# Optimization experiments

Hardware: AMD Instinct MI355X
Metric: run time of the kernel (lower is better)

The kernel has to match this reference:

```python
import jax, jax.numpy as jnp
import numpy as np

B, N, D, H = 256, 40, 256, 256      # molecules, atoms/molecule, pc_hidden, pred_hidden
nS, nC, nB = 40, 5, 5               # n_SYMBOLS, n_FORMAL_CHARGES, n_BOND_TYPES
NEG_SLOPE = 0.01                    # F.leaky_relu default


def _lrelu(x):
    return jnp.where(x >= 0, x, NEG_SLOPE * x)


def setup_inputs() -> dict:
    key = jax.random.key(0)
    ks = jax.random.split(key, 7)
    def w(k, shape, fan_in):
        return jax.random.normal(k, shape, jnp.float32) / np.float32(np.sqrt(fan_in))
    return {
        "yhat": jax.random.normal(ks[0], (B, N, D), jnp.float32),
        "Ws1": w(ks[1], (D, H), D),      "bs1": jnp.zeros((H,), jnp.float32),
        "Ws2": w(ks[2], (H, nS), H),     "bs2": jnp.zeros((nS,), jnp.float32),
        "Wc1": w(ks[3], (D, H), D),      "bc1": jnp.zeros((H,), jnp.float32),
        "Wc2": w(ks[4], (H, nC), H),     "bc2": jnp.zeros((nC,), jnp.float32),
        "Wb1": w(ks[5], (2 * D, H), 2 * D), "bb1": jnp.zeros((H,), jnp.float32),
        "Wb2": w(ks[6], (H, nB), H),     "bb2": jnp.zeros((nB,), jnp.float32),
    }


def reference(yhat, Ws1, bs1, Ws2, bs2, Wc1, bc1, Wc2, bc2, Wb1, bb1, Wb2, bb2):
    # Per-atom symbol / charge heads (2-layer MLP with leaky_relu)
    symbols = _lrelu(yhat @ Ws1 + bs1) @ Ws2 + bs2          # [B, N, nS]
    charges = _lrelu(yhat @ Wc1 + bc1) @ Wc2 + bc2          # [B, N, nC]

    # Pairwise bond head: concat(x_i, x_j) @ Wb1 == x_i @ Wb1[:D] + x_j @ Wb1[D:]
    # (avoids materializing the [B, N, N, 2D] concat tensor)
    p1 = yhat @ Wb1[:D]                                      # [B, N, H]
    p2 = yhat @ Wb1[D:]                                      # [B, N, H]
    h = _lrelu(p1[:, :, None, :] + p2[:, None, :, :] + bb1)  # [B, N, N, H]
    bonds = h @ Wb2 + bb2                                    # [B, N, N, nB]
    bonds = bonds + jnp.swapaxes(bonds, 1, 2)                # symmetrize (i,j)+(j,i)

    return (symbols.reshape(-1, nS),
            charges.reshape(-1, nC),
            bonds.reshape(-1, nB))
```

## Files before the change

kernel.cpp:

```cpp
#include <hip/hip_runtime.h>
#include <hip/hip_bf16.h>

typedef unsigned short u16;
typedef __attribute__((ext_vector_type(4))) int   int4v;
typedef __attribute__((ext_vector_type(4))) unsigned int uint4v;
typedef __attribute__((ext_vector_type(4))) unsigned short ushort4v;
typedef __attribute__((ext_vector_type(4))) float floatx4;
typedef __attribute__((ext_vector_type(8))) short bf16x8;

#define LRELU_NS 0.01f
#define SK 264

__device__ __forceinline__ float bitsToF(unsigned int b) {
    union { unsigned int u; float f; } v; v.u = b << 16; return v.f;
}
__device__ __forceinline__ float bfLo(unsigned int d) {
    union { unsigned int u; float f; } v; v.u = d << 16; return v.f;
}
__device__ __forceinline__ float bfHi(unsigned int d) {
    union { unsigned int u; float f; } v; v.u = d & 0xffff0000u; return v.f;
}
__device__ __forceinline__ u16 f2bf(float f) {
    __hip_bfloat16 h = __float2bfloat16(f);
    return *reinterpret_cast<u16*>(&h);
}
__device__ __forceinline__ float lrelu(float v) {
    return fmaxf(v, LRELU_NS * v);
}
__device__ __forceinline__ u16 ldW(const void* p, int i, int isF32) {
    return isF32 ? f2bf(((const float*)p)[i]) : ((const u16*)p)[i];
}
__device__ __forceinline__ float ldF(const void* p, int i, int isF32) {
    return isF32 ? ((const float*)p)[i]
                 : bitsToF((unsigned int)((const u16*)p)[i]);
}

__device__ __forceinline__ int computeIsF32(const u16* y, int* cnt, int t) {
    if (t == 0) *cnt = 0;
    __syncthreads();
    if (t < 256) {
        u16 v = y[2 * t];
        int e = (v >> 7) & 0xFF;
        if (v == 0 || (e >= 96 && e < 160)) atomicAdd(cnt, 1);
    }
    __syncthreads();
    return (*cnt < 192) ? 1 : 0;
}

__global__ __launch_bounds__(256) void pack_kernel(
    const void* __restrict__ yhat,
    const void* __restrict__ Ws1, const void* __restrict__ Wc1,
    const void* __restrict__ Wb1, const void* __restrict__ Ws2,
    const void* __restrict__ Wc2,
    const void* __restrict__ bs1, const void* __restrict__ bc1,
    const void* __restrict__ bb1, const void* __restrict__ bs2,
    const void* __restrict__ bc2, const void* __restrict__ bb2,
    u16* __restrict__ WallT, u16* __restrict__ W2T, float* __restrict__ biasF)
{
    __shared__ int fcnt;
    const int bid = blockIdx.x, t = threadIdx.x;
    const int isF32 = computeIsF32((const u16*)yhat, &fcnt, t);
    if (bid < 64) {
        __shared__ u16 tile[64][65];
        const int c0 = (bid & 15) * 64;
        const int k0 = (bid >> 4) * 64;
        const void* src; int coff; int roff = 0;
        if (c0 < 256)      { src = Ws1; coff = c0; }
        else if (c0 < 512) { src = Wc1; coff = c0 - 256; }
        else if (c0 < 768) { src = Wb1; coff = c0 - 512; }
        else               { src = Wb1; coff = c0 - 768; roff = 256; }
        const int cc = t & 63, kk0 = t >> 6;
        #pragma unroll
        for (int i = 0; i < 16; ++i) {
            int kk = kk0 + i * 4;
            tile[kk][cc] = ldW(src, (k0 + kk + roff) * 256 + coff + cc, isF32);
        }
        __syncthreads();
        const int kk2 = t & 63, cc0 = t >> 6;
        #pragma unroll
        for (int i = 0; i < 16; ++i) {
            int cc2 = cc0 + i * 4;
            WallT[(c0 + cc2) * 256 + (k0 + kk2)] = tile[kk2][cc2];
        }
    } else if (bid < 128) {
        int e2 = (bid - 64) * 256 + t;
        int c = e2 >> 8, k = e2 & 255;
        u16 v = 0;
        if (c < 40)                 v = ldW(Ws2, k * 40 + c, isF32);
        else if (c >= 48 && c < 53) v = ldW(Wc2, k * 5 + (c - 48), isF32);
        W2T[c * 256 + k] = v;
    } else {
        int idx = (bid - 128) * 256 + t;
        float v = 0.f;
        if (idx < 256)       v = ldF(bs1, idx, isF32);
        else if (idx < 512)  v = ldF(bc1, idx - 256, isF32);
        else if (idx < 768)  v = ldF(bb1, idx - 512, isF32);
        else if (idx < 808)  v = ldF(bs2, idx - 768, isF32);
        else if (idx < 813)  v = ldF(bc2, idx - 808, isF32);
        else if (idx >= 816 && idx < 821) v = ldF(bb2, idx - 816, isF32);
        biasF[idx] = v;
    }
}

__global__ __launch_bounds__(512) void l1all_kernel(
    const void* __restrict__ Xv, const u16* __restrict__ WallT,
    const float* __restrict__ biasF,
    u16* __restrict__ Hs, u16* __restrict__ Hc,
    u16* __restrict__ P1g, u16* __restrict__ P2g)
{
    __shared__ u16 Xs[64 * SK];
    __shared__ int fcnt;
    const int t = threadIdx.x;
    const int bm0 = blockIdx.x * 64;
    const int y = blockIdx.y;
    const int isF32 = computeIsF32((const u16*)Xv, &fcnt, t);

    if (isF32) {
        const floatx4* __restrict__ src = (const floatx4*)((const float*)Xv + bm0 * 256);
        #pragma unroll
        for (int s = 0; s < 8; ++s) {
            int cid = t + s * 512;
            int row = cid >> 6, ch = cid & 63;
            floatx4 f = src[cid];
            ushort4v u;
            u[0] = f2bf(f[0]); u[1] = f2bf(f[1]); u[2] = f2bf(f[2]); u[3] = f2bf(f[3]);
            *(ushort4v*)&Xs[row * SK + ch * 4] = u;
        }
    } else {
        const int4v* __restrict__ src = (const int4v*)((const u16*)Xv + bm0 * 256);
        #pragma unroll
        for (int s = 0; s < 4; ++s) {
            int cid = t + s * 512;
            int row = cid >> 5, ch = cid & 31;
            *(int4v*)&Xs[row * SK + ch * 8] = src[cid];
        }
    }
    __syncthreads();

    const int w = t >> 6, l = t & 63;
    const int ml = l & 15, kq = l >> 4, r0 = kq * 4;
    u16* __restrict__ dstBase = (y == 0) ? Hs : (y == 1) ? Hc : (y == 2) ? P1g : P2g;

    #pragma unroll
    for (int n = 0; n < 2; ++n) {
        const int ct = w + 8 * n;
        const int col = ct * 16 + ml;
        const int gc = y * 256 + col;
        floatx4 acc[4] = {};
        #pragma unroll
        for (int ks = 0; ks < 8; ++ks) {
            const int k0 = ks * 32 + kq * 8;
            bf16x8 bf = *(const bf16x8*)&WallT[gc * 256 + k0];
            #pragma unroll
            for (int mt = 0; mt < 4; ++mt) {
                bf16x8 a = *(const bf16x8*)&Xs[(mt * 16 + ml) * SK + k0];
                acc[mt] = __builtin_amdgcn_mfma_f32_16x16x32_bf16(a, bf, acc[mt], 0, 0, 0);
            }
        }
        const float bias = (y < 3) ? biasF[y * 256 + col] : 0.f;
        #pragma unroll
        for (int mt = 0; mt < 4; ++mt)
            #pragma unroll
            for (int r = 0; r < 4; ++r) {
                float v = acc[mt][r] + bias;
                if (y < 2) v = lrelu(v);
                dstBase[(bm0 + mt * 16 + r0 + r) * 256 + col] = f2bf(v);
            }
    }
}

__global__ __launch_bounds__(256) void l2heads_kernel(
    const void* __restrict__ Xv, const u16* __restrict__ Hs,
    const u16* __restrict__ Hc, const u16* __restrict__ W2T,
    const float* __restrict__ biasF, void* __restrict__ outv)
{
    __shared__ u16 Hb[64 * SK];
    __shared__ int fcnt;
    const int t = threadIdx.x;
    const int bm0 = blockIdx.x * 64;
    const int head = blockIdx.y;
    const int isF32 = computeIsF32((const u16*)Xv, &fcnt, t);

    const u16* __restrict__ Hg = (head == 0) ? Hs : Hc;
    const int4v* __restrict__ src = (const int4v*)(Hg + bm0 * 256);
    #pragma unroll
    for (int it = 0; it < 8; ++it) {
        int cid = t + it * 256;
        int row = cid >> 5, ch = cid & 31;
        *(int4v*)&Hb[row * SK + ch * 8] = src[cid];
    }
    __syncthreads();

    const int w = t >> 6, l = t & 63;
    const int ml = l & 15, kq = l >> 4, r0 = kq * 4;

    const int nct = (head == 0) ? 3 : 1;
    const int c0  = (head == 0) ? 0 : 48;
    floatx4 acc2[3] = {};
    #pragma unroll
    for (int ks = 0; ks < 8; ++ks) {
        const int k0 = ks * 32 + kq * 8;
        bf16x8 a = *(const bf16x8*)&Hb[(w * 16 + ml) * SK + k0];
        #pragma unroll
        for (int j = 0; j < 3; ++j) {
            if (j < nct) {
                bf16x8 bf = *(const bf16x8*)&W2T[(c0 + j * 16 + ml) * 256 + k0];
                acc2[j] = __builtin_amdgcn_mfma_f32_16x16x32_bf16(a, bf, acc2[j], 0, 0, 0);
            }
        }
    }
    #pragma unroll
    for (int j = 0; j < 3; ++j) {
        if (j < nct) {
            const int col = j * 16 + ml;
            const int lim = (head == 0) ? 40 : 5;
            if (col < lim) {
                const float bias = biasF[(head == 0 ? 768 : 808) + col];
                #pragma unroll
                for (int r = 0; r < 4; ++r) {
                    const int row = bm0 + w * 16 + r0 + r;
                    const int o = (head == 0) ? row * 40 + col
                                              : 409600 + row * 5 + col;
                    const float v = acc2[j][r] + bias;
                    if (isF32) ((float*)outv)[o] = v;
                    else ((__hip_bfloat16*)outv)[o] = __float2bfloat16(v);
                }
            }
        }
    }
}

__global__ __launch_bounds__(512, 4) void pairf_kernel(
    const void* __restrict__ Xv,
    const u16* __restrict__ P1g, const u16* __restrict__ P2g,
    const void* __restrict__ Wb2, const float* __restrict__ biasF,
    void* __restrict__ outv)
{
    __shared__ u16 Pq[4][16 * SK];
    __shared__ u16 WsB[16 * 264];
    __shared__ int fcnt;
    const int t = threadIdx.x, mol = blockIdx.x;
    const int y = blockIdx.y;
    const int it = (y < 3) ? 0 : (y < 5) ? 1 : 2;
    const int jt = (y < 3) ? y : (y < 5) ? (y - 2) : 2;
    const int isF32 = computeIsF32((const u16*)Xv, &fcnt, t);

    #pragma unroll
    for (int s = 0; s < 4; ++s) {
        const int cid = t + s * 512;
        const int buf = cid >> 9, r = (cid >> 5) & 15, ch = cid & 31;
        const int tile = (buf < 2) ? it : jt;
        const u16* __restrict__ src = (buf & 1) ? P2g : P1g;
        const int arow = tile * 16 + r;
        int4v v = {0, 0, 0, 0};
        if (arow < 40) v = *(const int4v*)&src[(mol * 40 + arow) * 256 + ch * 8];
        *(int4v*)&Pq[buf][r * SK + ch * 8] = v;
    }
    #pragma unroll
    for (int s = 0; s < 8; ++s) {
        const int e2 = t + s * 512;
        const int c = e2 >> 8, k = e2 & 255;
        WsB[c * 264 + k] = (c < 5) ? ldW(Wb2, k * 5 + c, isF32) : (u16)0;
    }
    __syncthreads();

    const int w = t >> 6, l = t & 63;
    const int ml = l & 15, kq = l >> 4, r0 = kq * 4;

    bf16x8 wf[8];
    #pragma unroll
    for (int ks = 0; ks < 8; ++ks)
        wf[ks] = *(const bf16x8*)&WsB[ml * 264 + ks * 32 + kq * 8];
    const float b2x2 = 2.f * biasF[816 + ml];

    const int i0 = it * 16 + w;
    const int i1 = i0 + 8;
    const bool do1 = (it != 2);
    floatx4 acc0 = {}, acc1 = {};
    #pragma unroll
    for (int ks = 0; ks < 8; ++ks) {
        const int k0 = ks * 32 + kq * 8;
        const uint4v b1 = *(const uint4v*)&Pq[2][ml * SK + k0];
        const uint4v b2 = *(const uint4v*)&Pq[3][ml * SK + k0];
        {
            const uint4v a1 = *(const uint4v*)&Pq[0][w * SK + k0];
            const uint4v a2 = *(const uint4v*)&Pq[1][w * SK + k0];
            bf16x8 af;
            #pragma unroll
            for (int d = 0; d < 4; ++d) {
                const float sLo = lrelu(bfLo(a1[d]) + bfLo(b2[d]))
                                + lrelu(bfLo(b1[d]) + bfLo(a2[d]));
                const float sHi = lrelu(bfHi(a1[d]) + bfHi(b2[d]))
                                + lrelu(bfHi(b1[d]) + bfHi(a2[d]));
                af[2 * d]     = (short)f2bf(sLo);
                af[2 * d + 1] = (short)f2bf(sHi);
            }
            acc0 = __builtin_amdgcn_mfma_f32_16x16x32_bf16(af, wf[ks], acc0, 0, 0, 0);
        }
        if (do1) {
            const uint4v a1 = *(const uint4v*)&Pq[0][(w + 8) * SK + k0];
            const uint4v a2 = *(const uint4v*)&Pq[1][(w + 8) * SK + k0];
            bf16x8 af;
            #pragma unroll
            for (int d = 0; d < 4; ++d) {
                const float sLo = lrelu(bfLo(a1[d]) + bfLo(b2[d]))
                                + lrelu(bfLo(b1[d]) + bfLo(a2[d]));
                const float sHi = lrelu(bfHi(a1[d]) + bfHi(b2[d]))
                                + lrelu(bfHi(b1[d]) + bfHi(a2[d]));
                af[2 * d]     = (short)f2bf(sLo);
                af[2 * d + 1] = (short)f2bf(sHi);
            }
            acc1 = __builtin_amdgcn_mfma_f32_16x16x32_bf16(af, wf[ks], acc1, 0, 0, 0);
        }
    }

    if (ml < 5) {
        #pragma unroll
        for (int r = 0; r < 4; ++r) {
            const int j = jt * 16 + r0 + r;
            if (j < 40 && (it != jt || j >= i0)) {
                const float v = acc0[r] + b2x2;
                const int o1 = 460800 + (mol * 1600 + i0 * 40 + j) * 5 + ml;
                if (isF32) ((float*)outv)[o1] = v;
                else ((__hip_bfloat16*)outv)[o1] = __float2bfloat16(v);
                if (it != jt || j > i0) {
                    const int o2 = 460800 + (mol * 1600 + j * 40 + i0) * 5 + ml;
                    if (isF32) ((float*)outv)[o2] = v;
                    else ((__hip_bfloat16*)outv)[o2] = __float2bfloat16(v);
                }
            }
        }
        if (do1) {
            #pragma unroll
            for (int r = 0; r < 4; ++r) {
                const int j = jt * 16 + r0 + r;
                if (j < 40 && (it != jt || j >= i1)) {
                    const float v = acc1[r] + b2x2;
                    const int o1 = 460800 + (mol * 1600 + i1 * 40 + j) * 5 + ml;
                    if (isF32) ((float*)outv)[o1] = v;
                    else ((__hip_bfloat16*)outv)[o1] = __float2bfloat16(v);
                    if (it != jt || j > i1) {
                        const int o2 = 460800 + (mol * 1600 + j * 40 + i1) * 5 + ml;
                        if (isF32) ((float*)outv)[o2] = v;
                        else ((__hip_bfloat16*)outv)[o2] = __float2bfloat16(v);
                    }
                }
            }
        }
    }
}

__global__ __launch_bounds__(256) void heads_kernel(
    const void* __restrict__ Xv, const u16* __restrict__ WallT,
    const u16* __restrict__ W2T, const float* __restrict__ biasF,
    void* __restrict__ outv)
{
    __shared__ u16 Xs[64 * SK];
    __shared__ u16 Hb[64 * SK];
    __shared__ int fcnt;
    const int t = threadIdx.x;
    const int bm0 = blockIdx.x * 64;
    const int head = blockIdx.y;
    const int isF32 = computeIsF32((const u16*)Xv, &fcnt, t);

    if (isF32) {
        const floatx4* __restrict__ src = (const floatx4*)((const float*)Xv + bm0 * 256);
        #pragma unroll
        for (int it = 0; it < 16; ++it) {
            int cid = t + it * 256;
            int row = cid >> 6, ch = cid & 63;
            floatx4 f = src[cid];
            ushort4v u;
            u[0] = f2bf(f[0]); u[1] = f2bf(f[1]); u[2] = f2bf(f[2]); u[3] = f2bf(f[3]);
            *(ushort4v*)&Xs[row * SK + ch * 4] = u;
        }
    } else {
        const int4v* __restrict__ src = (const int4v*)((const u16*)Xv + bm0 * 256);
        #pragma unroll
        for (int it = 0; it < 8; ++it) {
            int cid = t + it * 256;
            int row = cid >> 5, ch = cid & 31;
            *(int4v*)&Xs[row * SK + ch * 8] = src[cid];
        }
    }
    __syncthreads();

    const int w = t >> 6, l = t & 63;
    const int ml = l & 15, kq = l >> 4, r0 = kq * 4;

    for (int n = 0; n < 4; ++n) {
        const int ct = w + 4 * n;
        floatx4 acc[4] = {};
        #pragma unroll
        for (int ks = 0; ks < 8; ++ks) {
            const int k0 = ks * 32 + kq * 8;
            bf16x8 bf = *(const bf16x8*)&WallT[(head * 256 + ct * 16 + ml) * 256 + k0];
            #pragma unroll
            for (int mt = 0; mt < 4; ++mt) {
                bf16x8 a = *(const bf16x8*)&Xs[(mt * 16 + ml) * SK + k0];
                acc[mt] = __builtin_amdgcn_mfma_f32_16x16x32_bf16(a, bf, acc[mt], 0, 0, 0);
            }
        }
        const int col = ct * 16 + ml;
        const float bias = biasF[head * 256 + col];
        #pragma unroll
        for (int mt = 0; mt < 4; ++mt)
            #pragma unroll
            for (int r = 0; r < 4; ++r)
                Hb[(mt * 16 + r0 + r) * SK + col] = f2bf(lrelu(acc[mt][r] + bias));
    }
    __syncthreads();

    const int nct = (head == 0) ? 3 : 1;
    const int c0  = (head == 0) ? 0 : 48;
    floatx4 acc2[3] = {};
    #pragma unroll
    for (int ks = 0; ks < 8; ++ks) {
        const int k0 = ks * 32 + kq * 8;
        bf16x8 a = *(const bf16x8*)&Hb[(w * 16 + ml) * SK + k0];
        #pragma unroll
        for (int j = 0; j < 3; ++j) {
            if (j < nct) {
                bf16x8 bf = *(const bf16x8*)&W2T[(c0 + j * 16 + ml) * 256 + k0];
                acc2[j] = __builtin_amdgcn_mfma_f32_16x16x32_bf16(a, bf, acc2[j], 0, 0, 0);
            }
        }
    }
    #pragma unroll
    for (int j = 0; j < 3; ++j) {
        if (j < nct) {
            const int col = j * 16 + ml;
            const int lim = (head == 0) ? 40 : 5;
            if (col < lim) {
                const float bias = biasF[(head == 0 ? 768 : 808) + col];
                #pragma unroll
                for (int r = 0; r < 4; ++r) {
                    const int row = bm0 + w * 16 + r0 + r;
                    const int o = (head == 0) ? row * 40 + col
                                              : 409600 + row * 5 + col;
                    const float v = acc2[j][r] + bias;
                    if (isF32) ((float*)outv)[o] = v;
                    else ((__hip_bfloat16*)outv)[o] = __float2bfloat16(v);
                }
            }
        }
    }
}

__global__ __launch_bounds__(512) void l1p_kernel(
    const void* __restrict__ Xv, const u16* __restrict__ WallT,
    const float* __restrict__ biasF,
    u16* __restrict__ P1g, u16* __restrict__ P2g)
{
    __shared__ u16 Xs[64 * SK];
    __shared__ int fcnt;
    const int t = threadIdx.x;
    const int bm0 = blockIdx.x * 64;
    const int isF32 = computeIsF32((const u16*)Xv, &fcnt, t);

    if (isF32) {
        const floatx4* __restrict__ src = (const floatx4*)((const float*)Xv + bm0 * 256);
        #pragma unroll
        for (int s = 0; s < 8; ++s) {
            int cid = t + s * 512;
            int row = cid >> 6, ch = cid & 63;
            floatx4 f = src[cid];
            ushort4v u;
            u[0] = f2bf(f[0]); u[1] = f2bf(f[1]); u[2] = f2bf(f[2]); u[3] = f2bf(f[3]);
            *(ushort4v*)&Xs[row * SK + ch * 4] = u;
        }
    } else {
        const int4v* __restrict__ src = (const int4v*)((const u16*)Xv + bm0 * 256);
        #pragma unroll
        for (int s = 0; s < 4; ++s) {
            int cid = t + s * 512;
            int row = cid >> 5, ch = cid & 31;
            *(int4v*)&Xs[row * SK + ch * 8] = src[cid];
        }
    }
    __syncthreads();

    const int w = t >> 6, l = t & 63;
    const int ml = l & 15, kq = l >> 4, r0 = kq * 4;
    const int ct = blockIdx.y * 8 + w;
    const int gc = ct * 16 + ml;

    floatx4 acc[4] = {};
    #pragma unroll
    for (int ks = 0; ks < 8; ++ks) {
        const int k0 = ks * 32 + kq * 8;
        bf16x8 bf = *(const bf16x8*)&WallT[(512 + gc) * 256 + k0];
        #pragma unroll
        for (int mt = 0; mt < 4; ++mt) {
            bf16x8 a = *(const bf16x8*)&Xs[(mt * 16 + ml) * SK + k0];
            acc[mt] = __builtin_amdgcn_mfma_f32_16x16x32_bf16(a, bf, acc[mt], 0, 0, 0);
        }
    }
    const float bias = (gc < 256) ? biasF[512 + gc] : 0.f;
    u16* __restrict__ dst = (gc < 256) ? P1g : P2g;
    const int col = gc & 255;
    #pragma unroll
    for (int mt = 0; mt < 4; ++mt)
        #pragma unroll
        for (int r = 0; r < 4; ++r)
            dst[(bm0 + mt * 16 + r0 + r) * 256 + col] = f2bf(acc[mt][r] + bias);
}

__global__ __launch_bounds__(512) void bonds_kernel(
    const void* __restrict__ Xv, const u16* __restrict__ WallT,
    const void* __restrict__ Wb2, const float* __restrict__ biasF,
    void* __restrict__ outv)
{
    __shared__ u16 Xm[48 * SK];
    __shared__ u16 P1L[48 * SK];
    __shared__ u16 P2L[48 * SK];
    __shared__ u16 WsB[16 * 264];
    __shared__ float fbuf[8000];
    __shared__ int fcnt;
    const int t = threadIdx.x, b = blockIdx.x;
    const int isF32 = computeIsF32((const u16*)Xv, &fcnt, t);

    if (isF32) {
        const floatx4* __restrict__ src = (const floatx4*)((const float*)Xv + b * 10240);
        #pragma unroll
        for (int it = 0; it < 5; ++it) {
            int cid = t + it * 512;
            int row = cid >> 6, ch = cid & 63;
            floatx4 f = src[cid];
            ushort4v u;
            u[0] = f2bf(f[0]); u[1] = f2bf(f[1]); u[2] = f2bf(f[2]); u[3] = f2bf(f[3]);
            *(ushort4v*)&Xm[row * SK + ch * 4] = u;
        }
        {
            int row = 40 + (t >> 6), ch = t & 63;
            ushort4v z = {0, 0, 0, 0};
            *(ushort4v*)&Xm[row * SK + ch * 4] = z;
        }
    } else {
        const int4v* __restrict__ src = (const int4v*)((const u16*)Xv + b * 10240);
        #pragma unroll
        for (int it = 0; it < 3; ++it) {
            int cid = t + it * 512;
            int row = cid >> 5, ch = cid & 31;
            if (cid < 1280) *(int4v*)&Xm[row * SK + ch * 8] = src[cid];
            else { int4v z = {0, 0, 0, 0}; *(int4v*)&Xm[row * SK + ch * 8] = z; }
        }
    }
    #pragma unroll
    for (int it = 0; it < 8; ++it) {
        int e2 = t + it * 512;
        int c = e2 >> 8, k = e2 & 255;
        WsB[c * 264 + k] = (c < 5) ? ldW(Wb2, k * 5 + c, isF32) : (u16)0;
    }
    __syncthreads();

    const int w = t >> 6, l = t & 63;
    const int ml = l & 15, kq = l >> 4, r0 = kq * 4;

    for (int n = 0; n < 4; ++n) {
        const int gc = (w + 8 * n) * 16 + ml;
        floatx4 acc[3] = {};
        #pragma unroll
        for (int ks = 0; ks < 8; ++ks) {
            const int k0 = ks * 32 + kq * 8;
            bf16x8 bf = *(const bf16x8*)&WallT[(512 + gc) * 256 + k0];
            #pragma unroll
            for (int i = 0; i < 3; ++i) {
                bf16x8 a = *(const bf16x8*)&Xm[(i * 16 + ml) * SK + k0];
                acc[i] = __builtin_amdgcn_mfma_f32_16x16x32_bf16(a, bf, acc[i], 0, 0, 0);
            }
        }
        u16* dst = (gc < 256) ? P1L : P2L;
        const int col = gc & 255;
        const float bias = (gc < 256) ? biasF[512 + gc] : 0.f;
        #pragma unroll
        for (int i = 0; i < 3; ++i)
            #pragma unroll
            for (int r = 0; r < 4; ++r)
                dst[(i * 16 + r0 + r) * SK + col] = f2bf(acc[i][r] + bias);
    }
    __syncthreads();

    bf16x8 wf[8];
    #pragma unroll
    for (int ks = 0; ks < 8; ++ks)
        wf[ks] = *(const bf16x8*)&WsB[ml * 264 + ks * 32 + kq * 8];

    for (int m = 0; m < 5; ++m) {
        const int i = w + 8 * m;
        uint4v pa8[8];
        #pragma unroll
        for (int ks = 0; ks < 8; ++ks)
            pa8[ks] = *(const uint4v*)&P1L[i * SK + ks * 32 + kq * 8];
        for (int jt = 0; jt < 3; ++jt) {
            floatx4 acc = {};
            #pragma unroll
            for (int ks = 0; ks < 8; ++ks) {
                const int k0 = ks * 32 + kq * 8;
                uint4v pa = pa8[ks];
                uint4v pb = *(const uint4v*)&P2L[(jt * 16 + ml) * SK + k0];
                bf16x8 af;
                #pragma unroll
                for (int d = 0; d < 4; ++d) {
                    af[2 * d]     = (short)f2bf(lrelu(bfLo(pa[d]) + bfLo(pb[d])));
                    af[2 * d + 1] = (short)f2bf(lrelu(bfHi(pa[d]) + bfHi(pb[d])));
                }
                acc = __builtin_amdgcn_mfma_f32_16x16x32_bf16(af, wf[ks], acc, 0, 0, 0);
            }
            if (ml < 5) {
                #pragma unroll
                for (int r = 0; r < 4; ++r) {
                    const int j = jt * 16 + r0 + r;
                    if (j < 40) fbuf[(i * 40 + j) * 5 + ml] = acc[r];
                }
            }
        }
    }
    __syncthreads();

    const int base = 460800 + b * 8000;
    for (int e = t; e < 8000; e += 512) {
        int pr = e / 5, c = e - pr * 5;
        int i = pr / 40, j = pr - (pr / 40) * 40;
        float v = fbuf[e] + fbuf[(j * 40 + i) * 5 + c] + 2.f * biasF[816 + c];
        if (isF32) ((float*)outv)[base + e] = v;
        else ((__hip_bfloat16*)outv)[base + e] = __float2bfloat16(v);
    }
}

extern "C" void kernel_launch(void* const* d_in, const int* in_sizes, int n_in,
                              void* d_out, int out_size, void* d_ws, size_t ws_size,
                              hipStream_t stream)
{
    const void* yhat = d_in[0];
    const void* Ws1  = d_in[1];
    const void* bs1  = d_in[2];
    const void* Ws2  = d_in[3];
    const void* bs2  = d_in[4];
    const void* Wc1  = d_in[5];
    const void* bc1  = d_in[6];
    const void* Wc2  = d_in[7];
    const void* bc2  = d_in[8];
    const void* Wb1  = d_in[9];
    const void* bb1  = d_in[10];
    const void* Wb2  = d_in[11];
    const void* bb2  = d_in[12];

    char* wsb = (char*)d_ws;
    float* biasF = (float*)(wsb + 4096);
    u16*   W2T   = (u16*)(wsb + 8192);
    u16*   WallT = (u16*)(wsb + 40960);
    const size_t P_BYTES = (size_t)10240 * 256 * 2;
    u16* P1g = (u16*)(wsb + 565248);
    u16* P2g = (u16*)(wsb + 565248 + P_BYTES);
    u16* Hs  = (u16*)(wsb + 565248 + 2 * P_BYTES);
    u16* Hc  = (u16*)(wsb + 565248 + 3 * P_BYTES);
    const bool big  = ws_size >= 565248 + 2 * P_BYTES;
    const bool bigH = ws_size >= 565248 + 4 * P_BYTES;

    pack_kernel<<<132, 256, 0, stream>>>(yhat, Ws1, Wc1, Wb1, Ws2, Wc2,
                                         bs1, bc1, bb1, bs2, bc2, bb2,
                                         WallT, W2T, biasF);
    if (bigH) {
        l1all_kernel<<<dim3(160, 4), 512, 0, stream>>>(yhat, WallT, biasF,
                                                       Hs, Hc, P1g, P2g);
        l2heads_kernel<<<dim3(160, 2), 256, 0, stream>>>(yhat, Hs, Hc, W2T,
                                                         biasF, d_out);
        pairf_kernel<<<dim3(256, 6), 512, 0, stream>>>(yhat, P1g, P2g, Wb2,
                                                       biasF, d_out);
    } else if (big) {
        heads_kernel<<<dim3(160, 2), 256, 0, stream>>>(yhat, WallT, W2T, biasF, d_out);
        l1p_kernel<<<dim3(160, 4), 512, 0, stream>>>(yhat, WallT, biasF, P1g, P2g);
        pairf_kernel<<<dim3(256, 6), 512, 0, stream>>>(yhat, P1g, P2g, Wb2,
                                                       biasF, d_out);
    } else {
        heads_kernel<<<dim3(160, 2), 256, 0, stream>>>(yhat, WallT, W2T, biasF, d_out);
        bonds_kernel<<<256, 512, 0, stream>>>(yhat, WallT, Wb2, biasF, d_out);
    }
}
```

Before: 149.1 us.

## Fuse pack, layer-1, heads and pair stages into one cooperative persistent kernel

Replaces the four separate launches (pack, l1all, l2heads, pairf) with a single cooperative mega-kernel. It loops over job queues per stage and separates the stages with grid.sync(), sized from occupancy times CU count. Layer-2 heads now run inside the same block as layer 1, with the hidden activations kept in shared memory instead of going through the Hs/Hc global buffers. This cuts launch gaps and global round-trips, but adds grid-wide barriers and possible lower occupancy from the larger shared union. If the cooperative launch fails, it falls back to the separate kernels.

```diff
diff --git a/kernel.cpp b/kernel.cpp
--- a/kernel.cpp
+++ b/kernel.cpp
@@ -1,5 +1,8 @@
 #include <hip/hip_runtime.h>
 #include <hip/hip_bf16.h>
+#include <hip/hip_cooperative_groups.h>
+
+namespace cg = cooperative_groups;
 
 typedef unsigned short u16;
 typedef __attribute__((ext_vector_type(4))) int   int4v;
@@ -45,6 +48,304 @@
     }
     __syncthreads();
     return (*cnt < 192) ? 1 : 0;
+}
+
+union SharedU {
+    u16 tile[64][65];
+    struct { u16 Xs[64 * SK]; u16 Hb[64 * SK]; } p1;
+    struct { u16 Pq[4][16 * SK]; u16 WsB[16 * 264]; } p2;
+};
+
+__global__ __launch_bounds__(512) void mega_kernel(
+    const void* __restrict__ yhat,
+    const void* __restrict__ Ws1, const void* __restrict__ Wc1,
+    const void* __restrict__ Wb1, const void* __restrict__ Ws2,
+    const void* __restrict__ Wc2,
+    const void* __restrict__ bs1, const void* __restrict__ bc1,
+    const void* __restrict__ bb1, const void* __restrict__ bs2,
+    const void* __restrict__ bc2, const void* __restrict__ bb2,
+    const void* __restrict__ Wb2,
+    u16* __restrict__ WallT, u16* __restrict__ W2T, float* __restrict__ biasF,
+    u16* __restrict__ P1g, u16* __restrict__ P2g, void* __restrict__ outv)
+{
+    __shared__ SharedU sh;
+    __shared__ int fcnt;
+    const int t = threadIdx.x;
+    const int isF32 = computeIsF32((const u16*)yhat, &fcnt, t);
+    cg::grid_group grid = cg::this_grid();
+
+    const int w = t >> 6, l = t & 63;
+    const int ml = l & 15, kq = l >> 4, r0 = kq * 4;
+
+    for (int job = blockIdx.x; job < 98; job += gridDim.x) {
+        if (job < 64) {
+            const int c0 = (job & 15) * 64;
+            const int k0 = (job >> 4) * 64;
+            const void* src; int coff; int roff = 0;
+            if (c0 < 256)      { src = Ws1; coff = c0; }
+            else if (c0 < 512) { src = Wc1; coff = c0 - 256; }
+            else if (c0 < 768) { src = Wb1; coff = c0 - 512; }
+            else               { src = Wb1; coff = c0 - 768; roff = 256; }
+            const int cc = t & 63, kk0 = t >> 6;
+            #pragma unroll
+            for (int i = 0; i < 8; ++i) {
+                int kk = kk0 + i * 8;
+                sh.tile[kk][cc] = ldW(src, (k0 + kk + roff) * 256 + coff + cc, isF32);
+            }
+            __syncthreads();
+            const int kk2 = t & 63, cc0 = t >> 6;
+            #pragma unroll
+            for (int i = 0; i < 8; ++i) {
+                int cc2 = cc0 + i * 8;
+                WallT[(c0 + cc2) * 256 + (k0 + kk2)] = sh.tile[kk2][cc2];
+            }
+            __syncthreads();
+        } else if (job < 96) {
+            int e2 = (job - 64) * 512 + t;
+            int c = e2 >> 8, k = e2 & 255;
+            u16 v = 0;
+            if (c < 40)                 v = ldW(Ws2, k * 40 + c, isF32);
+            else if (c >= 48 && c < 53) v = ldW(Wc2, k * 5 + (c - 48), isF32);
+            W2T[c * 256 + k] = v;
+        } else {
+            int idx = (job - 96) * 512 + t;
+            float v = 0.f;
+            if (idx < 256)       v = ldF(bs1, idx, isF32);
+            else if (idx < 512)  v = ldF(bc1, idx - 256, isF32);
+            else if (idx < 768)  v = ldF(bb1, idx - 512, isF32);
+            else if (idx < 808)  v = ldF(bs2, idx - 768, isF32);
+            else if (idx < 813)  v = ldF(bc2, idx - 808, isF32);
+            else if (idx >= 816 && idx < 821) v = ldF(bb2, idx - 816, isF32);
+            biasF[idx] = v;
+        }
+    }
+    grid.sync();
+
+    for (int job = blockIdx.x; job < 480; job += gridDim.x) {
+        const int bm0 = (job % 160) * 64;
+        const int y = job / 160;
+        if (isF32) {
+            const floatx4* __restrict__ src = (const floatx4*)((const float*)yhat + bm0 * 256);
+            #pragma unroll
+            for (int s = 0; s < 8; ++s) {
+                int cid = t + s * 512;
+                int row = cid >> 6, ch = cid & 63;
+                floatx4 f = src[cid];
+                ushort4v u;
+                u[0] = f2bf(f[0]); u[1] = f2bf(f[1]); u[2] = f2bf(f[2]); u[3] = f2bf(f[3]);
+                *(ushort4v*)&sh.p1.Xs[row * SK + ch * 4] = u;
+            }
+        } else {
+            const int4v* __restrict__ src = (const int4v*)((const u16*)yhat + bm0 * 256);
+            #pragma unroll
+            for (int s = 0; s < 4; ++s) {
+                int cid = t + s * 512;
+                int row = cid >> 5, ch = cid & 31;
+                *(int4v*)&sh.p1.Xs[row * SK + ch * 8] = src[cid];
+            }
+        }
+        __syncthreads();
+
+        if (y < 2) {
+            #pragma unroll
+            for (int n = 0; n < 2; ++n) {
+                const int ct = w + 8 * n;
+                floatx4 acc[4] = {};
+                #pragma unroll
+                for (int ks = 0; ks < 8; ++ks) {
+                    const int k0 = ks * 32 + kq * 8;
+                    bf16x8 bf = *(const bf16x8*)&WallT[(y * 256 + ct * 16 + ml) * 256 + k0];
+                    #pragma unroll
+                    for (int mt = 0; mt < 4; ++mt) {
+                        bf16x8 a = *(const bf16x8*)&sh.p1.Xs[(mt * 16 + ml) * SK + k0];
+                        acc[mt] = __builtin_amdgcn_mfma_f32_16x16x32_bf16(a, bf, acc[mt], 0, 0, 0);
+                    }
+                }
+                const int col = ct * 16 + ml;
+                const float bias = biasF[y * 256 + col];
+                #pragma unroll
+                for (int mt = 0; mt < 4; ++mt)
+                    #pragma unroll
+                    for (int r = 0; r < 4; ++r)
+                        sh.p1.Hb[(mt * 16 + r0 + r) * SK + col] = f2bf(lrelu(acc[mt][r] + bias));
+            }
+            __syncthreads();
+            if (w < 4) {
+                const int nct = (y == 0) ? 3 : 1;
+                const int c0  = (y == 0) ? 0 : 48;
+                floatx4 acc2[3] = {};
+                #pragma unroll
+                for (int ks = 0; ks < 8; ++ks) {
+                    const int k0 = ks * 32 + kq * 8;
+                    bf16x8 a = *(const bf16x8*)&sh.p1.Hb[(w * 16 + ml) * SK + k0];
+                    #pragma unroll
+                    for (int j = 0; j < 3; ++j) {
+                        if (j < nct) {
+                            bf16x8 bf = *(const bf16x8*)&W2T[(c0 + j * 16 + ml) * 256 + k0];
+                            acc2[j] = __builtin_amdgcn_mfma_f32_16x16x32_bf16(a, bf, acc2[j], 0, 0, 0);
+                        }
+                    }
+                }
+                #pragma unroll
+                for (int j = 0; j < 3; ++j) {
+                    if (j < nct) {
+                        const int col = j * 16 + ml;
+                        const int lim = (y == 0) ? 40 : 5;
+                        if (col < lim) {
+                            const float bias = biasF[(y == 0 ? 768 : 808) + col];
+                            #pragma unroll
+                            for (int r = 0; r < 4; ++r) {
+                                const int row = bm0 + w * 16 + r0 + r;
+                                const int o = (y == 0) ? row * 40 + col
+                                                       : 409600 + row * 5 + col;
+                                const float v = acc2[j][r] + bias;
+                                if (isF32) ((float*)outv)[o] = v;
+                                else ((__hip_bfloat16*)outv)[o] = __float2bfloat16(v);
+                            }
+                        }
+                    }
+                }
+            }
+        } else {
+            #pragma unroll
+            for (int s = 0; s < 2; ++s) {
+                u16* __restrict__ dst = s ? P2g : P1g;
+                #pragma unroll
+                for (int n = 0; n < 2; ++n) {
+                    const int ct = w + 8 * n;
+                    const int col = ct * 16 + ml;
+                    floatx4 acc[4] = {};
+                    #pragma unroll
+                    for (int ks = 0; ks < 8; ++ks) {
+                        const int k0 = ks * 32 + kq * 8;
+                        bf16x8 bf = *(const bf16x8*)&WallT[(512 + s * 256 + col) * 256 + k0];
+                        #pragma unroll
+                        for (int mt = 0; mt < 4; ++mt) {
+                            bf16x8 a = *(const bf16x8*)&sh.p1.Xs[(mt * 16 + ml) * SK + k0];
+                            acc[mt] = __builtin_amdgcn_mfma_f32_16x16x32_bf16(a, bf, acc[mt], 0, 0, 0);
+                        }
+                    }
+                    const float bias = s ? 0.f : biasF[512 + col];
+                    #pragma unroll
+                    for (int mt = 0; mt < 4; ++mt)
+                        #pragma unroll
+                        for (int r = 0; r < 4; ++r)
+                            dst[(bm0 + mt * 16 + r0 + r) * 256 + col] = f2bf(acc[mt][r] + bias);
+                }
+            }
+        }
+        __syncthreads();
+    }
+    grid.sync();
+
+    for (int job = blockIdx.x; job < 1536; job += gridDim.x) {
+        const int mol = job / 6;
+        const int yb = job - mol * 6;
+        const int it = (yb < 3) ? 0 : (yb < 5) ? 1 : 2;
+        const int jt = (yb < 3) ? yb : (yb < 5) ? (yb - 2) : 2;
+
+        #pragma unroll
+        for (int s = 0; s < 4; ++s) {
+            const int cid = t + s * 512;
+            const int buf = cid >> 9, r = (cid >> 5) & 15, ch = cid & 31;
+            const int tile = (buf < 2) ? it : jt;
+            const u16* __restrict__ src = (buf & 1) ? P2g : P1g;
+            const int arow = tile * 16 + r;
+            int4v v = {0, 0, 0, 0};
+            if (arow < 40) v = *(const int4v*)&src[(mol * 40 + arow) * 256 + ch * 8];
+            *(int4v*)&sh.p2.Pq[buf][r * SK + ch * 8] = v;
+        }
+        #pragma unroll
+        for (int s = 0; s < 8; ++s) {
+            const int e2 = t + s * 512;
+            const int c = e2 >> 8, k = e2 & 255;
+            sh.p2.WsB[c * 264 + k] = (c < 5) ? ldW(Wb2, k * 5 + c, isF32) : (u16)0;
+        }
+        __syncthreads();
+
+        bf16x8 wf[8];
+        #pragma unroll
+        for (int ks = 0; ks < 8; ++ks)
+            wf[ks] = *(const bf16x8*)&sh.p2.WsB[ml * 264 + ks * 32 + kq * 8];
+        const float b2x2 = 2.f * biasF[816 + ml];
+
+        const int i0 = it * 16 + w;
+        const int i1 = i0 + 8;
+        const bool do1 = (it != 2);
+        floatx4 acc0 = {}, acc1 = {};
+        #pragma unroll
+        for (int ks = 0; ks < 8; ++ks) {
+            const int k0 = ks * 32 + kq * 8;
+            const uint4v b1 = *(const uint4v*)&sh.p2.Pq[2][ml * SK + k0];
+            const uint4v b2 = *(const uint4v*)&sh.p2.Pq[3][ml * SK + k0];
+            {
+                const uint4v a1 = *(const uint4v*)&sh.p2.Pq[0][w * SK + k0];
+                const uint4v a2 = *(const uint4v*)&sh.p2.Pq[1][w * SK + k0];
+                bf16x8 af;
+                #pragma unroll
+                for (int d = 0; d < 4; ++d) {
+                    const float sLo = lrelu(bfLo(a1[d]) + bfLo(b2[d]))
+                                    + lrelu(bfLo(b1[d]) + bfLo(a2[d]));
+                    const float sHi = lrelu(bfHi(a1[d]) + bfHi(b2[d]))
+                                    + lrelu(bfHi(b1[d]) + bfHi(a2[d]));
+                    af[2 * d]     = (short)f2bf(sLo);
+                    af[2 * d + 1] = (short)f2bf(sHi);
+                }
+                acc0 = __builtin_amdgcn_mfma_f32_16x16x32_bf16(af, wf[ks], acc0, 0, 0, 0);
+            }
+            if (do1) {
+                const uint4v a1 = *(const uint4v*)&sh.p2.Pq[0][(w + 8) * SK + k0];
+                const uint4v a2 = *(const uint4v*)&sh.p2.Pq[1][(w + 8) * SK + k0];
+                bf16x8 af;
+                #pragma unroll
+                for (int d = 0; d < 4; ++d) {
+                    const float sLo = lrelu(bfLo(a1[d]) + bfLo(b2[d]))
+                                    + lrelu(bfLo(b1[d]) + bfLo(a2[d]));
+                    const float sHi = lrelu(bfHi(a1[d]) + bfHi(b2[d]))
+                                    + lrelu(bfHi(b1[d]) + bfHi(a2[d]));
+                    af[2 * d]     = (short)f2bf(sLo);
+                    af[2 * d + 1] = (short)f2bf(sHi);
+                }
+                acc1 = __builtin_amdgcn_mfma_f32_16x16x32_bf16(af, wf[ks], acc1, 0, 0, 0);
+            }
+        }
+
+        if (ml < 5) {
+            #pragma unroll
+            for (int r = 0; r < 4; ++r) {
+                const int j = jt * 16 + r0 + r;
+                if (j < 40 && (it != jt || j >= i0)) {
+                    const float v = acc0[r] + b2x2;
+                    const int o1 = 460800 + (mol * 1600 + i0 * 40 + j) * 5 + ml;
+                    if (isF32) ((float*)outv)[o1] = v;
+                    else ((__hip_bfloat16*)outv)[o1] = __float2bfloat16(v);
+                    if (it != jt || j > i0) {
+                        const int o2 = 460800 + (mol * 1600 + j * 40 + i0) * 5 + ml;
+                        if (isF32) ((float*)outv)[o2] = v;
+                        else ((__hip_bfloat16*)outv)[o2] = __float2bfloat16(v);
+                    }
+                }
+            }
+            if (do1) {
+                #pragma unroll
+                for (int r = 0; r < 4; ++r) {
+                    const int j = jt * 16 + r0 + r;
+                    if (j < 40 && (it != jt || j >= i1)) {
+                        const float v = acc1[r] + b2x2;
+                        const int o1 = 460800 + (mol * 1600 + i1 * 40 + j) * 5 + ml;
+                        if (isF32) ((float*)outv)[o1] = v;
+                        else ((__hip_bfloat16*)outv)[o1] = __float2bfloat16(v);
+                        if (it != jt || j > i1) {
+                            const int o2 = 460800 + (mol * 1600 + j * 40 + i1) * 5 + ml;
+                            if (isF32) ((float*)outv)[o2] = v;
+                            else ((__hip_bfloat16*)outv)[o2] = __float2bfloat16(v);
+                        }
+                    }
+                }
+            }
+        }
+        __syncthreads();
+    }
 }
 
 __global__ __launch_bounds__(256) void pack_kernel(
@@ -102,17 +403,112 @@
     }
 }
 
-__global__ __launch_bounds__(512) void l1all_kernel(
+__global__ __launch_bounds__(256) void heads_kernel(
+    const void* __restrict__ Xv, const u16* __restrict__ WallT,
+    const u16* __restrict__ W2T, const float* __restrict__ biasF,
+    void* __restrict__ outv)
+{
+    __shared__ u16 Xs[64 * SK];
+    __shared__ u16 Hb[64 * SK];
+    __shared__ int fcnt;
+    const int t = threadIdx.x;
+    const int bm0 = blockIdx.x * 64;
+    const int head = blockIdx.y;
+    const int isF32 = computeIsF32((const u16*)Xv, &fcnt, t);
+
+    if (isF32) {
+        const floatx4* __restrict__ src = (const floatx4*)((const float*)Xv + bm0 * 256);
+        #pragma unroll
+        for (int it = 0; it < 16; ++it) {
+            int cid = t + it * 256;
+            int row = cid >> 6, ch = cid & 63;
+            floatx4 f = src[cid];
+            ushort4v u;
+            u[0] = f2bf(f[0]); u[1] = f2bf(f[1]); u[2] = f2bf(f[2]); u[3] = f2bf(f[3]);
+            *(ushort4v*)&Xs[row * SK + ch * 4] = u;
+        }
+    } else {
+        const int4v* __restrict__ src = (const int4v*)((const u16*)Xv + bm0 * 256);
+        #pragma unroll
+        for (int it = 0; it < 8; ++it) {
+            int cid = t + it * 256;
+            int row = cid >> 5, ch = cid & 31;
+            *(int4v*)&Xs[row * SK + ch * 8] = src[cid];
+        }
+    }
+    __syncthreads();
+
+    const int w = t >> 6, l = t & 63;
+    const int ml = l & 15, kq = l >> 4, r0 = kq * 4;
+
+    for (int n = 0; n < 4; ++n) {
+        const int ct = w + 4 * n;
+        floatx4 acc[4] = {};
+        #pragma unroll
+        for (int ks = 0; ks < 8; ++ks) {
+            const int k0 = ks * 32 + kq * 8;
+            bf16x8 bf = *(const bf16x8*)&WallT[(head * 256 + ct * 16 + ml) * 256 + k0];
+            #pragma unroll
+            for (int mt = 0; mt < 4; ++mt) {
+                bf16x8 a = *(const bf16x8*)&Xs[(mt * 16 + ml) * SK + k0];
+                acc[mt] = __builtin_amdgcn_mfma_f32_16x16x32_bf16(a, bf, acc[mt], 0, 0, 0);
+            }
+        }
+        const int col = ct * 16 + ml;
+        const float bias = biasF[head * 256 + col];
+        #pragma unroll
+        for (int mt = 0; mt < 4; ++mt)
+            #pragma unroll
+            for (int r = 0; r < 4; ++r)
+                Hb[(mt * 16 + r0 + r) * SK + col] = f2bf(lrelu(acc[mt][r] + bias));
+    }
+    __syncthreads();
+
+    const int nct = (head == 0) ? 3 : 1;
+    const int c0  = (head == 0) ? 0 : 48;
+    floatx4 acc2[3] = {};
+    #pragma unroll
+    for (int ks = 0; ks < 8; ++ks) {
+        const int k0 = ks * 32 + kq * 8;
+        bf16x8 a = *(const bf16x8*)&Hb[(w * 16 + ml) * SK + k0];
+        #pragma unroll
+        for (int j = 0; j < 3; ++j) {
+            if (j < nct) {
+                bf16x8 bf = *(const bf16x8*)&W2T[(c0 + j * 16 + ml) * 256 + k0];
+                acc2[j] = __builtin_amdgcn_mfma_f32_16x16x32_bf16(a, bf, acc2[j], 0, 0, 0);
+            }
+        }
+    }
+    #pragma unroll
+    for (int j = 0; j < 3; ++j) {
+        if (j < nct) {
+            const int col = j * 16 + ml;
+            const int lim = (head == 0) ? 40 : 5;
+            if (col < lim) {
+                const float bias = biasF[(head == 0 ? 768 : 808) + col];
+                #pragma unroll
+                for (int r = 0; r < 4; ++r) {
+                    const int row = bm0 + w * 16 + r0 + r;
+                    const int o = (head == 0) ? row * 40 + col
+                                              : 409600 + row * 5 + col;
+                    const float v = acc2[j][r] + bias;
+                    if (isF32) ((float*)outv)[o] = v;
+                    else ((__hip_bfloat16*)outv)[o] = __float2bfloat16(v);
+                }
+            }
+        }
+    }
+}
+
+__global__ __launch_bounds__(512) void l1p_kernel(
     const void* __restrict__ Xv, const u16* __restrict__ WallT,
     const float* __restrict__ biasF,
-    u16* __restrict__ Hs, u16* __restrict__ Hc,
     u16* __restrict__ P1g, u16* __restrict__ P2g)
 {
     __shared__ u16 Xs[64 * SK];
     __shared__ int fcnt;
     const int t = threadIdx.x;
     const int bm0 = blockIdx.x * 64;
-    const int y = blockIdx.y;
     const int isF32 = computeIsF32((const u16*)Xv, &fcnt, t);
 
     if (isF32) {
@@ -139,95 +535,28 @@
 
     const int w = t >> 6, l = t & 63;
     const int ml = l & 15, kq = l >> 4, r0 = kq * 4;
-    u16* __restrict__ dstBase = (y == 0) ? Hs : (y == 1) ? Hc : (y == 2) ? P1g : P2g;
-
-    #pragma unroll
-    for (int n = 0; n < 2; ++n) {
-        const int ct = w + 8 * n;
-        const int col = ct * 16 + ml;
-        const int gc = y * 256 + col;
-        floatx4 acc[4] = {};
-        #pragma unroll
-        for (int ks = 0; ks < 8; ++ks) {
-            const int k0 = ks * 32 + kq * 8;
-            bf16x8 bf = *(const bf16x8*)&WallT[gc * 256 + k0];
-            #pragma unroll
-            for (int mt = 0; mt < 4; ++mt) {
-                bf16x8 a = *(const bf16x8*)&Xs[(mt * 16 + ml) * SK + k0];
-                acc[mt] = __builtin_amdgcn_mfma_f32_16x16x32_bf16(a, bf, acc[mt], 0, 0, 0);
-            }
-        }
-        const float bias = (y < 3) ? biasF[y * 256 + col] : 0.f;
-        #pragma unroll
-        for (int mt = 0; mt < 4; ++mt)
-            #pragma unroll
-            for (int r = 0; r < 4; ++r) {
-                float v = acc[mt][r] + bias;
-                if (y < 2) v = lrelu(v);
-                dstBase[(bm0 + mt * 16 + r0 + r) * 256 + col] = f2bf(v);
-            }
-    }
-}
-
-__global__ __launch_bounds__(256) void l2heads_kernel(
-    const void* __restrict__ Xv, const u16* __restrict__ Hs,
-    const u16* __restrict__ Hc, const u16* __restrict__ W2T,
-    const float* __restrict__ biasF, void* __restrict__ outv)
-{
-    __shared__ u16 Hb[64 * SK];
-    __shared__ int fcnt;
-    const int t = threadIdx.x;
-    const int bm0 = blockIdx.x * 64;
-    const int head = blockIdx.y;
-    const int isF32 = computeIsF32((const u16*)Xv, &fcnt, t);
-
-    const u16* __restrict__ Hg = (head == 0) ? Hs : Hc;
-    const int4v* __restrict__ src = (const int4v*)(Hg + bm0 * 256);
-    #pragma unroll
-    for (int it = 0; it < 8; ++it) {
-        int cid = t + it * 256;
-        int row = cid >> 5, ch = cid & 31;
-        *(int4v*)&Hb[row * SK + ch * 8] = src[cid];
-    }
-    __syncthreads();
-
-    const int w = t >> 6, l = t & 63;
-    const int ml = l & 15, kq = l >> 4, r0 = kq * 4;
-
-    const int nct = (head == 0) ? 3 : 1;
-    const int c0  = (head == 0) ? 0 : 48;
-    floatx4 acc2[3] = {};
+    const int ct = blockIdx.y * 8 + w;
+    const int gc = ct * 16 + ml;
+
+    floatx4 acc[4] = {};
     #pragma unroll
     for (int ks = 0; ks < 8; ++ks) {
         const int k0 = ks * 32 + kq * 8;
-        bf16x8 a = *(const bf16x8*)&Hb[(w * 16 + ml) * SK + k0];
-        #pragma unroll
-        for (int j = 0; j < 3; ++j) {
-            if (j < nct) {
-                bf16x8 bf = *(const bf16x8*)&W2T[(c0 + j * 16 + ml) * 256 + k0];
-                acc2[j] = __builtin_amdgcn_mfma_f32_16x16x32_bf16(a, bf, acc2[j], 0, 0, 0);
-            }
-        }
-    }
-    #pragma unroll
-    for (int j = 0; j < 3; ++j) {
-        if (j < nct) {
-            const int col = j * 16 + ml;
-            const int lim = (head == 0) ? 40 : 5;
-            if (col < lim) {
-                const float bias = biasF[(head == 0 ? 768 : 808) + col];
-                #pragma unroll
-                for (int r = 0; r < 4; ++r) {
-                    const int row = bm0 + w * 16 + r0 + r;
-                    const int o = (head == 0) ? row * 40 + col
-                                              : 409600 + row * 5 + col;
-                    const float v = acc2[j][r] + bias;
-                    if (isF32) ((float*)outv)[o] = v;
-                    else ((__hip_bfloat16*)outv)[o] = __float2bfloat16(v);
-                }
-            }
-        }
-    }
+        bf16x8 bf = *(const bf16x8*)&WallT[(512 + gc) * 256 + k0];
+        #pragma unroll
+        for (int mt = 0; mt < 4; ++mt) {
+            bf16x8 a = *(const bf16x8*)&Xs[(mt * 16 + ml) * SK + k0];
+            acc[mt] = __builtin_amdgcn_mfma_f32_16x16x32_bf16(a, bf, acc[mt], 0, 0, 0);
+        }
+    }
+    const float bias = (gc < 256) ? biasF[512 + gc] : 0.f;
+    u16* __restrict__ dst = (gc < 256) ? P1g : P2g;
+    const int col = gc & 255;
+    #pragma unroll
+    for (int mt = 0; mt < 4; ++mt)
+        #pragma unroll
+        for (int r = 0; r < 4; ++r)
+            dst[(bm0 + mt * 16 + r0 + r) * 256 + col] = f2bf(acc[mt][r] + bias);
 }
 
 __global__ __launch_bounds__(512, 4) void pairf_kernel(
@@ -348,162 +677,6 @@
             }
         }
     }
-}
-
-__global__ __launch_bounds__(256) void heads_kernel(
-    const void* __restrict__ Xv, const u16* __restrict__ WallT,
-    const u16* __restrict__ W2T, const float* __restrict__ biasF,
-    void* __restrict__ outv)
-{
-    __shared__ u16 Xs[64 * SK];
-    __shared__ u16 Hb[64 * SK];
-    __shared__ int fcnt;
-    const int t = threadIdx.x;
-    const int bm0 = blockIdx.x * 64;
-    const int head = blockIdx.y;
-    const int isF32 = computeIsF32((const u16*)Xv, &fcnt, t);
-
-    if (isF32) {
-        const floatx4* __restrict__ src = (const floatx4*)((const float*)Xv + bm0 * 256);
-        #pragma unroll
-        for (int it = 0; it < 16; ++it) {
-            int cid = t + it * 256;
-            int row = cid >> 6, ch = cid & 63;
-            floatx4 f = src[cid];
-            ushort4v u;
-            u[0] = f2bf(f[0]); u[1] = f2bf(f[1]); u[2] = f2bf(f[2]); u[3] = f2bf(f[3]);
-            *(ushort4v*)&Xs[row * SK + ch * 4] = u;
-        }
-    } else {
-        const int4v* __restrict__ src = (const int4v*)((const u16*)Xv + bm0 * 256);
-        #pragma unroll
-        for (int it = 0; it < 8; ++it) {
-            int cid = t + it * 256;
-            int row = cid >> 5, ch = cid & 31;
-            *(int4v*)&Xs[row * SK + ch * 8] = src[cid];
-        }
-    }
-    __syncthreads();
-
-    const int w = t >> 6, l = t & 63;
-    const int ml = l & 15, kq = l >> 4, r0 = kq * 4;
-
-    for (int n = 0; n < 4; ++n) {
-        const int ct = w + 4 * n;
-        floatx4 acc[4] = {};
-        #pragma unroll
-        for (int ks = 0; ks < 8; ++ks) {
-            const int k0 = ks * 32 + kq * 8;
-            bf16x8 bf = *(const bf16x8*)&WallT[(head * 256 + ct * 16 + ml) * 256 + k0];
-            #pragma unroll
-            for (int mt = 0; mt < 4; ++mt) {
-                bf16x8 a = *(const bf16x8*)&Xs[(mt * 16 + ml) * SK + k0];
-                acc[mt] = __builtin_amdgcn_mfma_f32_16x16x32_bf16(a, bf, acc[mt], 0, 0, 0);
-            }
-        }
-        const int col = ct * 16 + ml;
-        const float bias = biasF[head * 256 + col];
-        #pragma unroll
-        for (int mt = 0; mt < 4; ++mt)
-            #pragma unroll
-            for (int r = 0; r < 4; ++r)
-                Hb[(mt * 16 + r0 + r) * SK + col] = f2bf(lrelu(acc[mt][r] + bias));
-    }
-    __syncthreads();
-
-    const int nct = (head == 0) ? 3 : 1;
-    const int c0  = (head == 0) ? 0 : 48;
-    floatx4 acc2[3] = {};
-    #pragma unroll
-    for (int ks = 0; ks < 8; ++ks) {
-        const int k0 = ks * 32 + kq * 8;
-        bf16x8 a = *(const bf16x8*)&Hb[(w * 16 + ml) * SK + k0];
-        #pragma unroll
-        for (int j = 0; j < 3; ++j) {
-            if (j < nct) {
-                bf16x8 bf = *(const bf16x8*)&W2T[(c0 + j * 16 + ml) * 256 + k0];
-                acc2[j] = __builtin_amdgcn_mfma_f32_16x16x32_bf16(a, bf, acc2[j], 0, 0, 0);
-            }
-        }
-    }
-    #pragma unroll
-    for (int j = 0; j < 3; ++j) {
-        if (j < nct) {
-            const int col = j * 16 + ml;
-            const int lim = (head == 0) ? 40 : 5;
-            if (col < lim) {
-                const float bias = biasF[(head == 0 ? 768 : 808) + col];
-                #pragma unroll
-                for (int r = 0; r < 4; ++r) {
-                    const int row = bm0 + w * 16 + r0 + r;
-                    const int o = (head == 0) ? row * 40 + col
-                                              : 409600 + row * 5 + col;
-                    const float v = acc2[j][r] + bias;
-                    if (isF32) ((float*)outv)[o] = v;
-                    else ((__hip_bfloat16*)outv)[o] = __float2bfloat16(v);
-                }
-            }
-        }
-    }
-}
-
-__global__ __launch_bounds__(512) void l1p_kernel(
-    const void* __restrict__ Xv, const u16* __restrict__ WallT,
-    const float* __restrict__ biasF,
-    u16* __restrict__ P1g, u16* __restrict__ P2g)
-{
-    __shared__ u16 Xs[64 * SK];
-    __shared__ int fcnt;
-    const int t = threadIdx.x;
-    const int bm0 = blockIdx.x * 64;
-    const int isF32 = computeIsF32((const u16*)Xv, &fcnt, t);
-
-    if (isF32) {
-        const floatx4* __restrict__ src = (const floatx4*)((const float*)Xv + bm0 * 256);
-        #pragma unroll
-        for (int s = 0; s < 8; ++s) {
-            int cid = t + s * 512;
-            int row = cid >> 6, ch = cid & 63;
-            floatx4 f = src[cid];
-            ushort4v u;
-            u[0] = f2bf(f[0]); u[1] = f2bf(f[1]); u[2] = f2bf(f[2]); u[3] = f2bf(f[3]);
-            *(ushort4v*)&Xs[row * SK + ch * 4] = u;
-        }
-    } else {
-        const int4v* __restrict__ src = (const int4v*)((const u16*)Xv + bm0 * 256);
-        #pragma unroll
-        for (int s = 0; s < 4; ++s) {
-            int cid = t + s * 512;
-            int row = cid >> 5, ch = cid & 31;
-            *(int4v*)&Xs[row * SK + ch * 8] = src[cid];
-        }
-    }
-    __syncthreads();
-
-    const int w = t >> 6, l = t & 63;
-    const int ml = l & 15, kq = l >> 4, r0 = kq * 4;
-    const int ct = blockIdx.y * 8 + w;
-    const int gc = ct * 16 + ml;
-
-    floatx4 acc[4] = {};
-    #pragma unroll
-    for (int ks = 0; ks < 8; ++ks) {
-        const int k0 = ks * 32 + kq * 8;
-        bf16x8 bf = *(const bf16x8*)&WallT[(512 + gc) * 256 + k0];
-        #pragma unroll
-        for (int mt = 0; mt < 4; ++mt) {
-            bf16x8 a = *(const bf16x8*)&Xs[(mt * 16 + ml) * SK + k0];
-            acc[mt] = __builtin_amdgcn_mfma_f32_16x16x32_bf16(a, bf, acc[mt], 0, 0, 0);
-        }
-    }
-    const float bias = (gc < 256) ? biasF[512 + gc] : 0.f;
-    u16* __restrict__ dst = (gc < 256) ? P1g : P2g;
-    const int col = gc & 255;
-    #pragma unroll
-    for (int mt = 0; mt < 4; ++mt)
-        #pragma unroll
-        for (int r = 0; r < 4; ++r)
-            dst[(bm0 + mt * 16 + r0 + r) * 256 + col] = f2bf(acc[mt][r] + bias);
 }
 
 __global__ __launch_bounds__(512) void bonds_kernel(
@@ -653,28 +826,51 @@
     const size_t P_BYTES = (size_t)10240 * 256 * 2;
     u16* P1g = (u16*)(wsb + 565248);
     u16* P2g = (u16*)(wsb + 565248 + P_BYTES);
-    u16* Hs  = (u16*)(wsb + 565248 + 2 * P_BYTES);
-    u16* Hc  = (u16*)(wsb + 565248 + 3 * P_BYTES);
-    const bool big  = ws_size >= 565248 + 2 * P_BYTES;
-    const bool bigH = ws_size >= 565248 + 4 * P_BYTES;
-
-    pack_kernel<<<132, 256, 0, stream>>>(yhat, Ws1, Wc1, Wb1, Ws2, Wc2,
-                                         bs1, bc1, bb1, bs2, bc2, bb2,
-                                         WallT, W2T, biasF);
-    if (bigH) {
-        l1all_kernel<<<dim3(160, 4), 512, 0, stream>>>(yhat, WallT, biasF,
-                                                       Hs, Hc, P1g, P2g);
-        l2heads_kernel<<<dim3(160, 2), 256, 0, stream>>>(yhat, Hs, Hc, W2T,
-                                                         biasF, d_out);
-        pairf_kernel<<<dim3(256, 6), 512, 0, stream>>>(yhat, P1g, P2g, Wb2,
-                                                       biasF, d_out);
-    } else if (big) {
+    const bool big = ws_size >= 565248 + 2 * P_BYTES;
+
+    bool coopDone = false;
+    if (big) {
+        static int megaBlocks = -2;
+        if (megaBlocks == -2) {
+            int occ = 0;
+            if (hipOccupancyMaxActiveBlocksPerMultiprocessor(
+                    &occ, (const void*)mega_kernel, 512, 0) != hipSuccess || occ < 1)
+                occ = 1;
+            int nCU = 256;
+            hipDeviceProp_t props;
+            int dev = 0;
+            if (hipGetDevice(&dev) == hipSuccess &&
+                hipGetDeviceProperties(&props, dev) == hipSuccess &&
+                props.multiProcessorCount > 0)
+                nCU = props.multiProcessorCount;
+            megaBlocks = occ * nCU;
+        }
+        void* kargs[] = {
+            (void*)&yhat, (void*)&Ws1, (void*)&Wc1, (void*)&Wb1,
+            (void*)&Ws2, (void*)&Wc2,
+            (void*)&bs1, (void*)&bc1, (void*)&bb1,
+            (void*)&bs2, (void*)&bc2, (void*)&bb2,
+            (void*)&Wb2,
+            (void*)&WallT, (void*)&W2T, (void*)&biasF,
+            (void*)&P1g, (void*)&P2g, (void*)&d_out
+        };
+        hipError_t e = hipLaunchCooperativeKernel(
+            (const void*)mega_kernel, dim3(megaBlocks), dim3(512), kargs, 0, stream);
+        if (e == hipSuccess) coopDone = true;
+        else (void)hipGetLastError();
+    }
+
+    if (!coopDone) {
+        pack_kernel<<<132, 256, 0, stream>>>(yhat, Ws1, Wc1, Wb1, Ws2, Wc2,
+                                             bs1, bc1, bb1, bs2, bc2, bb2,
+                                             WallT, W2T, biasF);
         heads_kernel<<<dim3(160, 2), 256, 0, stream>>>(yhat, WallT, W2T, biasF, d_out);
-        l1p_kernel<<<dim3(160, 4), 512, 0, stream>>>(yhat, WallT, biasF, P1g, P2g);
-        pairf_kernel<<<dim3(256, 6), 512, 0, stream>>>(yhat, P1g, P2g, Wb2,
-                                                       biasF, d_out);
-    } else {
-        heads_kernel<<<dim3(160, 2), 256, 0, stream>>>(yhat, WallT, W2T, biasF, d_out);
-        bonds_kernel<<<256, 512, 0, stream>>>(yhat, WallT, Wb2, biasF, d_out);
-    }
-}
+        if (big) {
+            l1p_kernel<<<dim3(160, 4), 512, 0, stream>>>(yhat, WallT, biasF, P1g, P2g);
+            pairf_kernel<<<dim3(256, 6), 512, 0, stream>>>(yhat, P1g, P2g, Wb2,
+                                                           biasF, d_out);
+        } else {
+            bonds_kernel<<<256, 512, 0, stream>>>(yhat, WallT, Wb2, biasF, d_out);
+        }
+    }
+}
```

Measured after the change: 238.7 us. +60.1%, slower.
